# Kernel tuning notes

Hardware: AMD Instinct MI355X
Metric: run time of the kernel (lower is better)

## Reference

```python
import jax, jax.numpy as jnp
import numpy as np

N_NODES = 40000
N_EDGES = 640000
D_IN, D_HID, D_OUT = 128, 128, 40


def _gcn_layer(x, src, dst, norm, W, b, n):
    # PyG GCNConv: h = x @ W; aggregate norm * h[src] at dst; add bias.
    h = x @ W
    msg = norm[:, None] * h[src]          # [E+N, d] gathered messages
    return jax.ops.segment_sum(msg, dst, num_segments=n) + b


def setup_inputs() -> dict:
    key = jax.random.key(0)
    ks = jax.random.split(key, 8)
    x = jax.random.normal(ks[0], (N_NODES, D_IN), dtype=jnp.float32)
    edge_index = jax.random.randint(ks[1], (2, N_EDGES), 0, N_NODES)
    s_in = 1.0 / np.sqrt(D_IN)
    s_hid = 1.0 / np.sqrt(D_HID)
    W1 = jax.random.normal(ks[2], (D_IN, D_HID), dtype=jnp.float32) * s_in
    b1 = jnp.zeros((D_HID,), dtype=jnp.float32)
    W2 = jax.random.normal(ks[3], (D_HID, D_HID), dtype=jnp.float32) * s_hid
    b2 = jnp.zeros((D_HID,), dtype=jnp.float32)
    W3 = jax.random.normal(ks[4], (D_HID, D_OUT), dtype=jnp.float32) * s_hid
    b3 = jnp.zeros((D_OUT,), dtype=jnp.float32)
    return {"x": x, "edge_index": edge_index, "W1": W1, "b1": b1,
            "W2": W2, "b2": b2, "W3": W3, "b3": b3}


def reference(x, edge_index, W1, b1, W2, b2, W3, b3):
    n = x.shape[0]
    src = edge_index[0].astype(jnp.int32)
    dst = edge_index[1].astype(jnp.int32)

    # --- GCN normalization with self-loops (PyG GCNConv defaults) ---
    loops = jnp.arange(n, dtype=jnp.int32)
    src2 = jnp.concatenate([src, loops])
    dst2 = jnp.concatenate([dst, loops])
    deg = jax.ops.segment_sum(jnp.ones_like(dst2, dtype=x.dtype), dst2,
                              num_segments=n)
    dis = jnp.where(deg > 0, jax.lax.rsqrt(deg), 0.0)
    norm = dis[src2] * dis[dst2]          # [E+N]

    h = jax.nn.relu(_gcn_layer(x, src2, dst2, norm, W1, b1, n))
    h = jax.nn.relu(_gcn_layer(h, src2, dst2, norm, W2, b2, n))
    out = _gcn_layer(h, src2, dst2, norm, W3, b3, n)

    # --- reg_loss = trace(A @ A), A = dense COO adjacency (dupes summed) ---
    # trace(A@A) = sum_{i,j} A[i,j] * A[j,i]
    #            = sum over edge instances (i,j) of multiplicity of (j,i).
    # Computed sparsely via sorted key lookup instead of NxN densification.
    keys = src * n + dst                  # unique int32 key per (i,j)
    skeys = jnp.sort(keys)
    rev = dst * n + src
    lo = jnp.searchsorted(skeys, rev, side="left")
    hi = jnp.searchsorted(skeys, rev, side="right")
    reg_loss = jnp.sum((hi - lo).astype(jnp.float32))

    return jax.nn.log_softmax(out, axis=1), reg_loss
```

## Files before the change

kernel.cpp:

```cpp
#include <hip/hip_runtime.h>
#include <hip/hip_bf16.h>
#include <math.h>

#define NN 40000
#define EE 640000
#define CAP 64
#define MPAD 40064
#define LDS_STRIDE 136
#define FP8_STRIDE 144
#define E4B 625
#define NB 157

typedef short bf16x8 __attribute__((ext_vector_type(8)));
typedef float f32x16 __attribute__((ext_vector_type(16)));
typedef float f32x2 __attribute__((ext_vector_type(2)));

__device__ __forceinline__ unsigned bf16rne(float x) {
  unsigned u = __float_as_uint(x);
  return (u + 0x7fffu + ((u >> 16) & 1u)) >> 16;
}
__device__ __forceinline__ unsigned packbf2(float lo, float hi) {
  return bf16rne(lo) | (bf16rne(hi) << 16);
}
__device__ __forceinline__ float dis_of(const int* cnt, int i) {
  return rsqrtf((float)(cnt[i] + 1));
}
__device__ __forceinline__ f32x2 cvt2lo(unsigned u) {
  return __builtin_amdgcn_cvt_pk_f32_fp8((int)u, false);
}
__device__ __forceinline__ f32x2 cvt2hi(unsigned u) {
  return __builtin_amdgcn_cvt_pk_f32_fp8((int)u, true);
}
__device__ __forceinline__ unsigned char f32_to_fp8(float x) {
  return (unsigned char)(__builtin_amdgcn_cvt_pk_fp8_f32(x, x, 0, false) & 0xff);
}

__global__ __launch_bounds__(256) void edge_w_kernel(
    const int4* __restrict__ src4, const int4* __restrict__ dst4,
    int* __restrict__ cnt, unsigned short* __restrict__ csr,
    const float* __restrict__ W1, const float* __restrict__ W2,
    const float* __restrict__ W3, unsigned short* __restrict__ Wt1,
    unsigned short* __restrict__ Wt2, unsigned short* __restrict__ W3t,
    unsigned* __restrict__ Xb32, unsigned* __restrict__ H1b32) {
  int blk = blockIdx.x, t = threadIdx.x;
  if (blk < E4B) {
    int e = blk * 256 + t;
    int4 s = src4[e];
    int4 d = dst4[e];
    int p0 = atomicAdd(&cnt[d.x], 1);
    int p1 = atomicAdd(&cnt[d.y], 1);
    int p2 = atomicAdd(&cnt[d.z], 1);
    int p3 = atomicAdd(&cnt[d.w], 1);
    if (p0 < CAP) csr[d.x * CAP + p0] = (unsigned short)s.x;
    if (p1 < CAP) csr[d.y * CAP + p1] = (unsigned short)s.y;
    if (p2 < CAP) csr[d.z * CAP + p2] = (unsigned short)s.z;
    if (p3 < CAP) csr[d.w * CAP + p3] = (unsigned short)s.w;
  } else if (blk < 753) {
    bool is1 = blk < 689;
    int n = (blk - (is1 ? 625 : 689)) * 2 + (t >> 7);
    int k = t & 127;
    const float* W = is1 ? W1 : W2;
    unsigned short* Wt = is1 ? Wt1 : Wt2;
    Wt[n * 128 + k] = (unsigned short)bf16rne(W[k * 128 + n]);
  } else if (blk < 785) {
    int n = (blk - 753) * 2 + (t >> 7);
    int k = t & 127;
    float v = (n < 40) ? W3[k * 40 + n] : 0.f;
    W3t[n * 128 + k] = (unsigned short)bf16rne(v);
  } else {
    if (t < 32) Xb32[(size_t)NN * 32 + t] = 0u;
    else if (t < 64) H1b32[(size_t)NN * 32 + (t - 32)] = 0u;
  }
}

__global__ __launch_bounds__(256) void fill_x_kernel(
    const int* __restrict__ cnt, unsigned short* __restrict__ csr,
    const float4* __restrict__ X, uint2* __restrict__ Xb8v) {
  int blk = blockIdx.x, t = threadIdx.x;
  if (blk < NB) {
    int i = blk * 256 + t;
    if (i >= NN) return;
    int cn = cnt[i];
    cn = cn > CAP ? CAP : cn;
    int en = (cn + 7) & ~7;
    for (int k = cn; k < en; k++) csr[i * CAP + k] = (unsigned short)NN;
  } else {
    int i = (blk - NB) * 256 + t;
    float di = dis_of(cnt, i >> 4);
    float4 a = X[i * 2], b = X[i * 2 + 1];
    int lo = __builtin_amdgcn_cvt_pk_fp8_f32(di * a.x, di * a.y, 0, false);
    lo = __builtin_amdgcn_cvt_pk_fp8_f32(di * a.z, di * a.w, lo, true);
    int hi = __builtin_amdgcn_cvt_pk_fp8_f32(di * b.x, di * b.y, 0, false);
    hi = __builtin_amdgcn_cvt_pk_fp8_f32(di * b.z, di * b.w, hi, true);
    uint2 o;
    o.x = (unsigned)lo;
    o.y = (unsigned)hi;
    Xb8v[i] = o;
  }
}

__device__ __forceinline__ void agg128_body8(
    int node, int sub, const unsigned char* __restrict__ Hb,
    const int* __restrict__ cnt, const unsigned short* __restrict__ csr,
    unsigned* __restrict__ outB) {
  float di = dis_of(cnt, node);
  const unsigned char* Hbs = Hb + sub * 16;
  f32x2 a[8];
  {
    uint4 v = *(const uint4*)&Hbs[(size_t)node * 128];
    a[0] = cvt2lo(v.x);
    a[1] = cvt2hi(v.x);
    a[2] = cvt2lo(v.y);
    a[3] = cvt2hi(v.y);
    a[4] = cvt2lo(v.z);
    a[5] = cvt2hi(v.z);
    a[6] = cvt2lo(v.w);
    a[7] = cvt2hi(v.w);
  }
  int beg = node * CAP;
  int cn = cnt[node];
  cn = cn > CAP ? CAP : cn;
  int end = beg + ((cn + 7) & ~7);
  if (beg < end) {
    uint4 cs = *(const uint4*)&csr[beg];
    for (int e = beg; e < end; e += 8) {
      int s0 = cs.x & 0xffff, s1 = cs.x >> 16;
      int s2 = cs.y & 0xffff, s3 = cs.y >> 16;
      int s4 = cs.z & 0xffff, s5 = cs.z >> 16;
      int s6 = cs.w & 0xffff, s7 = cs.w >> 16;
      uint4 v0 = *(const uint4*)&Hbs[(size_t)s0 * 128];
      uint4 v1 = *(const uint4*)&Hbs[(size_t)s1 * 128];
      uint4 v2 = *(const uint4*)&Hbs[(size_t)s2 * 128];
      uint4 v3 = *(const uint4*)&Hbs[(size_t)s3 * 128];
      uint4 v4 = *(const uint4*)&Hbs[(size_t)s4 * 128];
      uint4 v5 = *(const uint4*)&Hbs[(size_t)s5 * 128];
      uint4 v6 = *(const uint4*)&Hbs[(size_t)s6 * 128];
      uint4 v7 = *(const uint4*)&Hbs[(size_t)s7 * 128];
      if (e + 8 < end) cs = *(const uint4*)&csr[e + 8];
#define ACC8(vv)                                    \
  a[0] += cvt2lo(vv.x); a[1] += cvt2hi(vv.x);       \
  a[2] += cvt2lo(vv.y); a[3] += cvt2hi(vv.y);       \
  a[4] += cvt2lo(vv.z); a[5] += cvt2hi(vv.z);       \
  a[6] += cvt2lo(vv.w); a[7] += cvt2hi(vv.w);
      ACC8(v0);
      ACC8(v1);
      ACC8(v2);
      ACC8(v3);
      ACC8(v4);
      ACC8(v5);
      ACC8(v6);
      ACC8(v7);
#undef ACC8
    }
  }
  unsigned o0 = packbf2(di * a[0].x, di * a[0].y);
  unsigned o1 = packbf2(di * a[1].x, di * a[1].y);
  unsigned o2 = packbf2(di * a[2].x, di * a[2].y);
  unsigned o3 = packbf2(di * a[3].x, di * a[3].y);
  unsigned o4 = packbf2(di * a[4].x, di * a[4].y);
  unsigned o5 = packbf2(di * a[5].x, di * a[5].y);
  unsigned o6 = packbf2(di * a[6].x, di * a[6].y);
  unsigned o7 = packbf2(di * a[7].x, di * a[7].y);
  *(uint4*)&outB[(size_t)node * 64 + sub * 8] = make_uint4(o0, o1, o2, o3);
  *(uint4*)&outB[(size_t)node * 64 + sub * 8 + 4] = make_uint4(o4, o5, o6, o7);
}

__global__ __launch_bounds__(256) void agg1_reg(
    const unsigned char* __restrict__ Xb8, const int* __restrict__ cnt,
    const unsigned short* __restrict__ csr, unsigned* __restrict__ outB,
    const int* __restrict__ src, const int* __restrict__ dst,
    float* __restrict__ out_scalar) {
  int blk = blockIdx.x, t = threadIdx.x;
  if (blk % 3 == 0) {
    int node = (blk / 3) * 32 + (t >> 3);
    agg128_body8(node, t & 7, Xb8, cnt, csr, outB);
    return;
  }
  int e = (blk - blk / 3 - 1) * 256 + t;
  int c = 0;
  {
    int i = src[e];
    unsigned j = (unsigned)dst[e];
    int cn = cnt[i];
    cn = cn > CAP ? CAP : cn;
    int q0 = (i * CAP) >> 3, q1 = q0 + (((cn + 7) & ~7) >> 3);
    const uint4* base = (const uint4*)csr;
    for (int q = q0; q < q1; q++) {
      uint4 v = base[q];
      c += ((v.x & 0xffffu) == j) + ((v.x >> 16) == j);
      c += ((v.y & 0xffffu) == j) + ((v.y >> 16) == j);
      c += ((v.z & 0xffffu) == j) + ((v.z >> 16) == j);
      c += ((v.w & 0xffffu) == j) + ((v.w >> 16) == j);
    }
  }
  float v = (float)c;
  for (int off = 32; off; off >>= 1) v += __shfl_down(v, off, 64);
  __shared__ float ws[4];
  int lane = threadIdx.x & 63, w = threadIdx.x >> 6;
  if (lane == 0) ws[w] = v;
  __syncthreads();
  if (threadIdx.x == 0) atomicAdd(out_scalar, ws[0] + ws[1] + ws[2] + ws[3]);
}

__global__ __launch_bounds__(256) void agg128b(
    const unsigned char* __restrict__ Hb8, const int* __restrict__ cnt,
    const unsigned short* __restrict__ csr, unsigned* __restrict__ outB) {
  int node = blockIdx.x * 32 + (threadIdx.x >> 3);
  agg128_body8(node, threadIdx.x & 7, Hb8, cnt, csr, outB);
}

__global__ __launch_bounds__(256) void gemm_mfma(
    const unsigned* __restrict__ Ab, const unsigned* __restrict__ Wt,
    const float* __restrict__ bias, const int* __restrict__ cnt,
    unsigned char* __restrict__ outB8) {
  __shared__ unsigned short At[128 * LDS_STRIDE];
  __shared__ unsigned short Bt[128 * LDS_STRIDE];
  __shared__ float dsh[128];
  int t = threadIdx.x;
  int rowBase = blockIdx.x * 128;
  if (t < 128) {
    int rr = rowBase + t;
    dsh[t] = (rr < NN) ? dis_of(cnt, rr) : 0.f;
  }
  {
    const uint4* ga = (const uint4*)(Ab + (size_t)rowBase * 64);
    const uint4* gw = (const uint4*)Wt;
#pragma unroll
    for (int i = 0; i < 8; i++) {
      int idx = i * 256 + t;
      int r = idx >> 4, c = idx & 15;
      uint4 va = ga[idx];
      uint4 vw = gw[idx];
      *(uint4*)&At[r * LDS_STRIDE + c * 8] = va;
      *(uint4*)&Bt[r * LDS_STRIDE + c * 8] = vw;
    }
  }
  __syncthreads();
  int lane = t & 63, w = t >> 6;
  int m31 = lane & 31;
  int khalf = (lane >> 5) * 8;
  f32x16 acc[4] = {};
#pragma unroll
  for (int ks = 0; ks < 8; ks++) {
    bf16x8 a = *(bf16x8*)&At[(w * 32 + m31) * LDS_STRIDE + ks * 16 + khalf];
#pragma unroll
    for (int nt = 0; nt < 4; nt++) {
      bf16x8 b = *(bf16x8*)&Bt[(nt * 32 + m31) * LDS_STRIDE + ks * 16 + khalf];
      acc[nt] = __builtin_amdgcn_mfma_f32_32x32x16_bf16(a, b, acc[nt], 0, 0, 0);
    }
  }
  __syncthreads();
  unsigned char* Ac = (unsigned char*)At;
  int rsel = (lane >> 5) * 4;
#pragma unroll
  for (int nt = 0; nt < 4; nt++) {
    int col = nt * 32 + m31;
    float bv = bias[col];
#pragma unroll
    for (int r = 0; r < 16; r++) {
      int rl = w * 32 + (r & 3) + 8 * (r >> 2) + rsel;
      float x = fmaxf(acc[nt][r] + bv, 0.f);
      Ac[rl * FP8_STRIDE + col] = f32_to_fp8(dsh[rl] * x);
    }
  }
  __syncthreads();
  {
#pragma unroll
    for (int i = 0; i < 4; i++) {
      int idx = i * 256 + t;
      int r = idx >> 3, c = idx & 7;
      int grow = rowBase + r;
      if (grow < NN) {
        uint4 vv = *(const uint4*)&Ac[r * FP8_STRIDE + c * 16];
        *(uint4*)&outB8[(size_t)grow * 128 + c * 16] = vv;
      }
    }
  }
}

__global__ __launch_bounds__(256) void gemm_mfma2(
    const unsigned* __restrict__ Ab, const unsigned* __restrict__ Wt,
    const float* __restrict__ bias, const int* __restrict__ cnt,
    const unsigned short* __restrict__ W3t, float* __restrict__ G3) {
  __shared__ unsigned short At[128 * LDS_STRIDE];
  __shared__ unsigned short Bt[128 * LDS_STRIDE];
  __shared__ float dsh[128];
  int t = threadIdx.x;
  int rowBase = blockIdx.x * 128;
  if (blockIdx.x == 0 && t < 40) G3[(size_t)NN * 40 + t] = 0.f;
  if (t < 128) {
    int rr = rowBase + t;
    dsh[t] = (rr < NN) ? dis_of(cnt, rr) : 0.f;
  }
  {
    const uint4* ga = (const uint4*)(Ab + (size_t)rowBase * 64);
    const uint4* gw = (const uint4*)Wt;
#pragma unroll
    for (int i = 0; i < 8; i++) {
      int idx = i * 256 + t;
      int r = idx >> 4, c = idx & 15;
      uint4 va = ga[idx];
      uint4 vw = gw[idx];
      *(uint4*)&At[r * LDS_STRIDE + c * 8] = va;
      *(uint4*)&Bt[r * LDS_STRIDE + c * 8] = vw;
    }
  }
  __syncthreads();
  int lane = t & 63, w = t >> 6;
  int m31 = lane & 31;
  int khalf = (lane >> 5) * 8;
  f32x16 acc[4] = {};
#pragma unroll
  for (int ks = 0; ks < 8; ks++) {
    bf16x8 a = *(bf16x8*)&At[(w * 32 + m31) * LDS_STRIDE + ks * 16 + khalf];
#pragma unroll
    for (int nt = 0; nt < 4; nt++) {
      bf16x8 b = *(bf16x8*)&Bt[(nt * 32 + m31) * LDS_STRIDE + ks * 16 + khalf];
      acc[nt] = __builtin_amdgcn_mfma_f32_32x32x16_bf16(a, b, acc[nt], 0, 0, 0);
    }
  }
  __syncthreads();
  int rsel = (lane >> 5) * 4;
#pragma unroll
  for (int nt = 0; nt < 4; nt++) {
    int col = nt * 32 + m31;
    float bv = bias[col];
#pragma unroll
    for (int r = 0; r < 16; r++) {
      int rl = w * 32 + (r & 3) + 8 * (r >> 2) + rsel;
      float x = fmaxf(acc[nt][r] + bv, 0.f);
      At[rl * LDS_STRIDE + col] = (unsigned short)bf16rne(dsh[rl] * x);
    }
  }
  {
    const uint4* gw3 = (const uint4*)W3t;
#pragma unroll
    for (int i = 0; i < 4; i++) {
      int idx = i * 256 + t;
      int r = idx >> 4, c = idx & 15;
      *(uint4*)&Bt[r * LDS_STRIDE + c * 8] = gw3[idx];
    }
  }
  __syncthreads();
  f32x16 acc2[2] = {};
#pragma unroll
  for (int ks = 0; ks < 8; ks++) {
    bf16x8 a = *(bf16x8*)&At[(w * 32 + m31) * LDS_STRIDE + ks * 16 + khalf];
#pragma unroll
    for (int nt = 0; nt < 2; nt++) {
      bf16x8 b = *(bf16x8*)&Bt[(nt * 32 + m31) * LDS_STRIDE + ks * 16 + khalf];
      acc2[nt] = __builtin_amdgcn_mfma_f32_32x32x16_bf16(a, b, acc2[nt], 0, 0, 0);
    }
  }
  __syncthreads();
  float* Gst = (float*)At;
#pragma unroll
  for (int nt = 0; nt < 2; nt++) {
    int col = nt * 32 + m31;
    if (col < 40) {
#pragma unroll
      for (int r = 0; r < 16; r++) {
        int rl = w * 32 + (r & 3) + 8 * (r >> 2) + rsel;
        Gst[rl * 40 + col] = acc2[nt][r];
      }
    }
  }
  __syncthreads();
  {
    int lim = NN - rowBase;
    int lim4 = (lim >= 128) ? 1280 : lim * 10;
#pragma unroll
    for (int i = 0; i < 5; i++) {
      int idx = i * 256 + t;
      if (idx < lim4) {
        float4 vv = *(const float4*)&Gst[idx * 4];
        *(float4*)&G3[(size_t)rowBase * 40 + idx * 4] = vv;
      }
    }
  }
}

__global__ __launch_bounds__(256) void agg40_softmax(
    const float* __restrict__ G, const int* __restrict__ cnt,
    const unsigned short* __restrict__ csr, const float* __restrict__ b3,
    float* __restrict__ outp) {
  int node = __builtin_amdgcn_readfirstlane(blockIdx.x * 4 + (threadIdx.x >> 6));
  int lane = threadIdx.x & 63;
  int cl = lane < 40 ? lane : 39;
  float di = dis_of(cnt, node);
  float a = G[(size_t)node * 40 + cl];
  int beg = node * CAP;
  int cn = cnt[node];
  cn = cn > CAP ? CAP : cn;
  int end = beg + ((cn + 7) & ~7);
  if (beg < end) {
    uint4 cs = *(const uint4*)&csr[beg];
    for (int e = beg; e < end; e += 8) {
      int s0 = cs.x & 0xffff, s1 = cs.x >> 16;
      int s2 = cs.y & 0xffff, s3 = cs.y >> 16;
      int s4 = cs.z & 0xffff, s5 = cs.z >> 16;
      int s6 = cs.w & 0xffff, s7 = cs.w >> 16;
      float g0 = G[(size_t)s0 * 40 + cl];
      float g1 = G[(size_t)s1 * 40 + cl];
      float g2 = G[(size_t)s2 * 40 + cl];
      float g3 = G[(size_t)s3 * 40 + cl];
      float g4 = G[(size_t)s4 * 40 + cl];
      float g5 = G[(size_t)s5 * 40 + cl];
      float g6 = G[(size_t)s6 * 40 + cl];
      float g7 = G[(size_t)s7 * 40 + cl];
      if (e + 8 < end) cs = *(const uint4*)&csr[e + 8];
      a += g0 + g1 + g2 + g3 + g4 + g5 + g6 + g7;
    }
  }
  float o = di * a + b3[cl];
  float m = (lane < 40) ? o : -1e30f;
  for (int off = 32; off; off >>= 1) m = fmaxf(m, __shfl_xor(m, off, 64));
  float ex = (lane < 40) ? expf(o - m) : 0.f;
  float ssum = ex;
  for (int off = 32; off; off >>= 1) ssum += __shfl_xor(ssum, off, 64);
  float res = o - m - logf(ssum);
  if (lane < 40) outp[(size_t)node * 40 + lane] = res;
}

extern "C" void kernel_launch(void* const* d_in, const int* in_sizes, int n_in,
                              void* d_out, int out_size, void* d_ws,
                              size_t ws_size, hipStream_t stream) {
  const float* X = (const float*)d_in[0];
  const int* ei = (const int*)d_in[1];
  const float* W1 = (const float*)d_in[2];
  const float* b1 = (const float*)d_in[3];
  const float* W2 = (const float*)d_in[4];
  const float* b2 = (const float*)d_in[5];
  const float* W3 = (const float*)d_in[6];
  const float* b3 = (const float*)d_in[7];
  float* out = (float*)d_out;

  const int* src = ei;
  const int* dst = ei + EE;

  char* w = (char*)d_ws;
  auto carve = [&](size_t bytes) {
    char* p = w;
    w += (bytes + 255) & ~(size_t)255;
    return p;
  };
  int* cnt = (int*)carve(NN * 4);
  unsigned short* csr = (unsigned short*)carve((size_t)NN * CAP * 2);
  unsigned short* Wt1 = (unsigned short*)carve(128 * 128 * 2);
  unsigned short* Wt2 = (unsigned short*)carve(128 * 128 * 2);
  unsigned short* W3t = (unsigned short*)carve(64 * 128 * 2);
  unsigned* Ab = (unsigned*)carve((size_t)MPAD * 128 * 2);
  char* blk = carve(((size_t)NN + 1) * 40 * 4 + ((size_t)NN + 1) * 128 * 2);
  unsigned char* Xb8 = (unsigned char*)blk;
  unsigned char* H1b8 = (unsigned char*)blk + ((size_t)NN + 1) * 128;
  float* G3 = (float*)blk;

  (void)hipMemsetAsync(cnt, 0, NN * 4, stream);
  (void)hipMemsetAsync((char*)d_out + (size_t)NN * 40 * 4, 0, 4, stream);

  const int GB = MPAD / 128;

  edge_w_kernel<<<786, 256, 0, stream>>>((const int4*)src, (const int4*)dst,
                                         cnt, csr, W1, W2, W3, Wt1, Wt2, W3t,
                                         (unsigned*)Xb8, (unsigned*)H1b8);
  fill_x_kernel<<<NB + 2500, 256, 0, stream>>>(cnt, csr, (const float4*)X,
                                               (uint2*)Xb8);
  agg1_reg<<<3750, 256, 0, stream>>>(Xb8, cnt, csr, Ab, src, dst,
                                     out + (size_t)NN * 40);
  gemm_mfma<<<GB, 256, 0, stream>>>(Ab, (const unsigned*)Wt1, b1, cnt, H1b8);
  agg128b<<<1250, 256, 0, stream>>>(H1b8, cnt, csr, Ab);
  gemm_mfma2<<<GB, 256, 0, stream>>>(Ab, (const unsigned*)Wt2, b2, cnt, W3t,
                                     G3);
  agg40_softmax<<<NN / 4, 256, 0, stream>>>(G3, cnt, csr, b3, out);
}
```

Baseline: 210.1 us.

## Split fp8 feature tables into column halves and restructure aggregation and reg-loss scheduling

Stores the fp8 node feature tables as two 64-byte column halves (A/B), and the aggregation kernel processes one half per block. Block indices are interleaved so groups of four blocks share a half, which should keep the gathered working set (about 2.5MB per half) cache-resident. CSR tail padding is replaced with in-loop masking to the dummy zero row, which removes the csr padding pass. The reg-loss edge counting moves into the fp8 conversion kernel, using masked tail handling. Outputs use nontemporal stores. In exchange there are more blocks, doubled index decode work per node, and extra select instructions.

```diff
diff --git a/kernel.cpp b/kernel.cpp
--- a/kernel.cpp
+++ b/kernel.cpp
@@ -9,11 +9,11 @@
 #define LDS_STRIDE 136
 #define FP8_STRIDE 144
 #define E4B 625
-#define NB 157
 
 typedef short bf16x8 __attribute__((ext_vector_type(8)));
 typedef float f32x16 __attribute__((ext_vector_type(16)));
 typedef float f32x2 __attribute__((ext_vector_type(2)));
+typedef unsigned u32x4 __attribute__((ext_vector_type(4)));
 
 __device__ __forceinline__ unsigned bf16rne(float x) {
   unsigned u = __float_as_uint(x);
@@ -41,7 +41,8 @@
     const float* __restrict__ W1, const float* __restrict__ W2,
     const float* __restrict__ W3, unsigned short* __restrict__ Wt1,
     unsigned short* __restrict__ Wt2, unsigned short* __restrict__ W3t,
-    unsigned* __restrict__ Xb32, unsigned* __restrict__ H1b32) {
+    unsigned* __restrict__ XbA32, unsigned* __restrict__ XbB32,
+    unsigned* __restrict__ HA32, unsigned* __restrict__ HB32) {
   int blk = blockIdx.x, t = threadIdx.x;
   if (blk < E4B) {
     int e = blk * 256 + t;
@@ -68,25 +69,23 @@
     float v = (n < 40) ? W3[k * 40 + n] : 0.f;
     W3t[n * 128 + k] = (unsigned short)bf16rne(v);
   } else {
-    if (t < 32) Xb32[(size_t)NN * 32 + t] = 0u;
-    else if (t < 64) H1b32[(size_t)NN * 32 + (t - 32)] = 0u;
+    if (t < 16) XbA32[(size_t)NN * 16 + t] = 0u;
+    else if (t < 32) XbB32[(size_t)NN * 16 + (t - 16)] = 0u;
+    else if (t < 48) HA32[(size_t)NN * 16 + (t - 32)] = 0u;
+    else if (t < 64) HB32[(size_t)NN * 16 + (t - 48)] = 0u;
   }
 }
 
 __global__ __launch_bounds__(256) void fill_x_kernel(
-    const int* __restrict__ cnt, unsigned short* __restrict__ csr,
-    const float4* __restrict__ X, uint2* __restrict__ Xb8v) {
+    const int* __restrict__ cnt, const float4* __restrict__ X,
+    uint2* __restrict__ XbA2, uint2* __restrict__ XbB2,
+    const unsigned short* __restrict__ csr, const int* __restrict__ src,
+    const int* __restrict__ dst, float* __restrict__ out_scalar) {
   int blk = blockIdx.x, t = threadIdx.x;
-  if (blk < NB) {
-    int i = blk * 256 + t;
-    if (i >= NN) return;
-    int cn = cnt[i];
-    cn = cn > CAP ? CAP : cn;
-    int en = (cn + 7) & ~7;
-    for (int k = cn; k < en; k++) csr[i * CAP + k] = (unsigned short)NN;
-  } else {
-    int i = (blk - NB) * 256 + t;
-    float di = dis_of(cnt, i >> 4);
+  if ((blk & 1) == 0) {
+    int i = (blk >> 1) * 256 + t;
+    int row = i >> 4, li = i & 15;
+    float di = dis_of(cnt, row);
     float4 a = X[i * 2], b = X[i * 2 + 1];
     int lo = __builtin_amdgcn_cvt_pk_fp8_f32(di * a.x, di * a.y, 0, false);
     lo = __builtin_amdgcn_cvt_pk_fp8_f32(di * a.z, di * a.w, lo, true);
@@ -95,103 +94,37 @@
     uint2 o;
     o.x = (unsigned)lo;
     o.y = (unsigned)hi;
-    Xb8v[i] = o;
-  }
-}
-
-__device__ __forceinline__ void agg128_body8(
-    int node, int sub, const unsigned char* __restrict__ Hb,
-    const int* __restrict__ cnt, const unsigned short* __restrict__ csr,
-    unsigned* __restrict__ outB) {
-  float di = dis_of(cnt, node);
-  const unsigned char* Hbs = Hb + sub * 16;
-  f32x2 a[8];
-  {
-    uint4 v = *(const uint4*)&Hbs[(size_t)node * 128];
-    a[0] = cvt2lo(v.x);
-    a[1] = cvt2hi(v.x);
-    a[2] = cvt2lo(v.y);
-    a[3] = cvt2hi(v.y);
-    a[4] = cvt2lo(v.z);
-    a[5] = cvt2hi(v.z);
-    a[6] = cvt2lo(v.w);
-    a[7] = cvt2hi(v.w);
-  }
-  int beg = node * CAP;
-  int cn = cnt[node];
-  cn = cn > CAP ? CAP : cn;
-  int end = beg + ((cn + 7) & ~7);
-  if (beg < end) {
-    uint4 cs = *(const uint4*)&csr[beg];
-    for (int e = beg; e < end; e += 8) {
-      int s0 = cs.x & 0xffff, s1 = cs.x >> 16;
-      int s2 = cs.y & 0xffff, s3 = cs.y >> 16;
-      int s4 = cs.z & 0xffff, s5 = cs.z >> 16;
-      int s6 = cs.w & 0xffff, s7 = cs.w >> 16;
-      uint4 v0 = *(const uint4*)&Hbs[(size_t)s0 * 128];
-      uint4 v1 = *(const uint4*)&Hbs[(size_t)s1 * 128];
-      uint4 v2 = *(const uint4*)&Hbs[(size_t)s2 * 128];
-      uint4 v3 = *(const uint4*)&Hbs[(size_t)s3 * 128];
-      uint4 v4 = *(const uint4*)&Hbs[(size_t)s4 * 128];
-      uint4 v5 = *(const uint4*)&Hbs[(size_t)s5 * 128];
-      uint4 v6 = *(const uint4*)&Hbs[(size_t)s6 * 128];
-      uint4 v7 = *(const uint4*)&Hbs[(size_t)s7 * 128];
-      if (e + 8 < end) cs = *(const uint4*)&csr[e + 8];
-#define ACC8(vv)                                    \
-  a[0] += cvt2lo(vv.x); a[1] += cvt2hi(vv.x);       \
-  a[2] += cvt2lo(vv.y); a[3] += cvt2hi(vv.y);       \
-  a[4] += cvt2lo(vv.z); a[5] += cvt2hi(vv.z);       \
-  a[6] += cvt2lo(vv.w); a[7] += cvt2hi(vv.w);
-      ACC8(v0);
-      ACC8(v1);
-      ACC8(v2);
-      ACC8(v3);
-      ACC8(v4);
-      ACC8(v5);
-      ACC8(v6);
-      ACC8(v7);
-#undef ACC8
-    }
-  }
-  unsigned o0 = packbf2(di * a[0].x, di * a[0].y);
-  unsigned o1 = packbf2(di * a[1].x, di * a[1].y);
-  unsigned o2 = packbf2(di * a[2].x, di * a[2].y);
-  unsigned o3 = packbf2(di * a[3].x, di * a[3].y);
-  unsigned o4 = packbf2(di * a[4].x, di * a[4].y);
-  unsigned o5 = packbf2(di * a[5].x, di * a[5].y);
-  unsigned o6 = packbf2(di * a[6].x, di * a[6].y);
-  unsigned o7 = packbf2(di * a[7].x, di * a[7].y);
-  *(uint4*)&outB[(size_t)node * 64 + sub * 8] = make_uint4(o0, o1, o2, o3);
-  *(uint4*)&outB[(size_t)node * 64 + sub * 8 + 4] = make_uint4(o4, o5, o6, o7);
-}
-
-__global__ __launch_bounds__(256) void agg1_reg(
-    const unsigned char* __restrict__ Xb8, const int* __restrict__ cnt,
-    const unsigned short* __restrict__ csr, unsigned* __restrict__ outB,
-    const int* __restrict__ src, const int* __restrict__ dst,
-    float* __restrict__ out_scalar) {
-  int blk = blockIdx.x, t = threadIdx.x;
-  if (blk % 3 == 0) {
-    int node = (blk / 3) * 32 + (t >> 3);
-    agg128_body8(node, t & 7, Xb8, cnt, csr, outB);
+    if (li < 8) XbA2[row * 8 + li] = o;
+    else XbB2[row * 8 + (li - 8)] = o;
     return;
   }
-  int e = (blk - blk / 3 - 1) * 256 + t;
+  int e = (blk >> 1) * 256 + t;
   int c = 0;
   {
     int i = src[e];
     unsigned j = (unsigned)dst[e];
     int cn = cnt[i];
     cn = cn > CAP ? CAP : cn;
-    int q0 = (i * CAP) >> 3, q1 = q0 + (((cn + 7) & ~7) >> 3);
-    const uint4* base = (const uint4*)csr;
-    for (int q = q0; q < q1; q++) {
+    const uint4* base = (const uint4*)&csr[i * CAP];
+    int full = cn >> 3;
+    for (int q = 0; q < full; q++) {
       uint4 v = base[q];
       c += ((v.x & 0xffffu) == j) + ((v.x >> 16) == j);
       c += ((v.y & 0xffffu) == j) + ((v.y >> 16) == j);
       c += ((v.z & 0xffffu) == j) + ((v.z >> 16) == j);
       c += ((v.w & 0xffffu) == j) + ((v.w >> 16) == j);
     }
+    int rem = cn & 7;
+    if (rem) {
+      uint4 v = base[full];
+      c += (int)((v.x & 0xffffu) == j);
+      c += ((v.x >> 16) == j) & (rem > 1);
+      c += ((v.y & 0xffffu) == j) & (rem > 2);
+      c += ((v.y >> 16) == j) & (rem > 3);
+      c += ((v.z & 0xffffu) == j) & (rem > 4);
+      c += ((v.z >> 16) == j) & (rem > 5);
+      c += ((v.w & 0xffffu) == j) & (rem > 6);
+    }
   }
   float v = (float)c;
   for (int off = 32; off; off >>= 1) v += __shfl_down(v, off, 64);
@@ -202,17 +135,81 @@
   if (threadIdx.x == 0) atomicAdd(out_scalar, ws[0] + ws[1] + ws[2] + ws[3]);
 }
 
-__global__ __launch_bounds__(256) void agg128b(
-    const unsigned char* __restrict__ Hb8, const int* __restrict__ cnt,
-    const unsigned short* __restrict__ csr, unsigned* __restrict__ outB) {
-  int node = blockIdx.x * 32 + (threadIdx.x >> 3);
-  agg128_body8(node, threadIdx.x & 7, Hb8, cnt, csr, outB);
+__global__ __launch_bounds__(256) void agg64(
+    const unsigned char* __restrict__ TA, const unsigned char* __restrict__ TB,
+    const int* __restrict__ cnt, const unsigned short* __restrict__ csr,
+    unsigned* __restrict__ outB) {
+  int blk = blockIdx.x, t = threadIdx.x;
+  int r = blk & 7;
+  int half = (r >> 2) & 1;
+  int nb = (blk >> 3) * 4 + (r & 3);
+  if (nb >= 1250) return;
+  int node = nb * 32 + (t >> 3);
+  int sub = t & 7;
+  const unsigned char* Hbs = (half ? TB : TA) + sub * 8;
+  float di = dis_of(cnt, node);
+  f32x2 a0, a1, a2, a3;
+  {
+    uint2 v = *(const uint2*)&Hbs[(size_t)node * 64];
+    a0 = cvt2lo(v.x);
+    a1 = cvt2hi(v.x);
+    a2 = cvt2lo(v.y);
+    a3 = cvt2hi(v.y);
+  }
+  int cn = cnt[node];
+  cn = cn > CAP ? CAP : cn;
+  const unsigned short* row = &csr[node * CAP];
+  if (cn > 0) {
+    uint4 cs = *(const uint4*)row;
+    for (int e = 0; e < cn; e += 8) {
+      int rem = cn - e;
+      int s0 = cs.x & 0xffff, s1 = cs.x >> 16;
+      int s2 = cs.y & 0xffff, s3 = cs.y >> 16;
+      int s4 = cs.z & 0xffff, s5 = cs.z >> 16;
+      int s6 = cs.w & 0xffff, s7 = cs.w >> 16;
+      s1 = rem > 1 ? s1 : NN;
+      s2 = rem > 2 ? s2 : NN;
+      s3 = rem > 3 ? s3 : NN;
+      s4 = rem > 4 ? s4 : NN;
+      s5 = rem > 5 ? s5 : NN;
+      s6 = rem > 6 ? s6 : NN;
+      s7 = rem > 7 ? s7 : NN;
+      uint2 v0 = *(const uint2*)&Hbs[(size_t)s0 * 64];
+      uint2 v1 = *(const uint2*)&Hbs[(size_t)s1 * 64];
+      uint2 v2 = *(const uint2*)&Hbs[(size_t)s2 * 64];
+      uint2 v3 = *(const uint2*)&Hbs[(size_t)s3 * 64];
+      uint2 v4 = *(const uint2*)&Hbs[(size_t)s4 * 64];
+      uint2 v5 = *(const uint2*)&Hbs[(size_t)s5 * 64];
+      uint2 v6 = *(const uint2*)&Hbs[(size_t)s6 * 64];
+      uint2 v7 = *(const uint2*)&Hbs[(size_t)s7 * 64];
+      if (e + 8 < cn) cs = *(const uint4*)&row[e + 8];
+#define ACC2(vv)                                    \
+  a0 += cvt2lo(vv.x); a1 += cvt2hi(vv.x);           \
+  a2 += cvt2lo(vv.y); a3 += cvt2hi(vv.y);
+      ACC2(v0);
+      ACC2(v1);
+      ACC2(v2);
+      ACC2(v3);
+      ACC2(v4);
+      ACC2(v5);
+      ACC2(v6);
+      ACC2(v7);
+#undef ACC2
+    }
+  }
+  u32x4 o;
+  o.x = packbf2(di * a0.x, di * a0.y);
+  o.y = packbf2(di * a1.x, di * a1.y);
+  o.z = packbf2(di * a2.x, di * a2.y);
+  o.w = packbf2(di * a3.x, di * a3.y);
+  __builtin_nontemporal_store(
+      o, (u32x4*)&outB[(size_t)node * 64 + half * 32 + sub * 4]);
 }
 
 __global__ __launch_bounds__(256) void gemm_mfma(
     const unsigned* __restrict__ Ab, const unsigned* __restrict__ Wt,
     const float* __restrict__ bias, const int* __restrict__ cnt,
-    unsigned char* __restrict__ outB8) {
+    unsigned char* __restrict__ HA8, unsigned char* __restrict__ HB8) {
   __shared__ unsigned short At[128 * LDS_STRIDE];
   __shared__ unsigned short Bt[128 * LDS_STRIDE];
   __shared__ float dsh[128];
@@ -272,7 +269,10 @@
       int grow = rowBase + r;
       if (grow < NN) {
         uint4 vv = *(const uint4*)&Ac[r * FP8_STRIDE + c * 16];
-        *(uint4*)&outB8[(size_t)grow * 128 + c * 16] = vv;
+        if (c < 4)
+          *(uint4*)&HA8[(size_t)grow * 64 + c * 16] = vv;
+        else
+          *(uint4*)&HB8[(size_t)grow * 64 + (c - 4) * 16] = vv;
       }
     }
   }
@@ -389,17 +389,24 @@
   int cl = lane < 40 ? lane : 39;
   float di = dis_of(cnt, node);
   float a = G[(size_t)node * 40 + cl];
-  int beg = node * CAP;
   int cn = cnt[node];
   cn = cn > CAP ? CAP : cn;
-  int end = beg + ((cn + 7) & ~7);
-  if (beg < end) {
-    uint4 cs = *(const uint4*)&csr[beg];
-    for (int e = beg; e < end; e += 8) {
+  const unsigned short* row = &csr[node * CAP];
+  if (cn > 0) {
+    uint4 cs = *(const uint4*)row;
+    for (int e = 0; e < cn; e += 8) {
+      int rem = cn - e;
       int s0 = cs.x & 0xffff, s1 = cs.x >> 16;
       int s2 = cs.y & 0xffff, s3 = cs.y >> 16;
       int s4 = cs.z & 0xffff, s5 = cs.z >> 16;
       int s6 = cs.w & 0xffff, s7 = cs.w >> 16;
+      s1 = rem > 1 ? s1 : NN;
+      s2 = rem > 2 ? s2 : NN;
+      s3 = rem > 3 ? s3 : NN;
+      s4 = rem > 4 ? s4 : NN;
+      s5 = rem > 5 ? s5 : NN;
+      s6 = rem > 6 ? s6 : NN;
+      s7 = rem > 7 ? s7 : NN;
       float g0 = G[(size_t)s0 * 40 + cl];
       float g1 = G[(size_t)s1 * 40 + cl];
       float g2 = G[(size_t)s2 * 40 + cl];
@@ -408,7 +415,7 @@
       float g5 = G[(size_t)s5 * 40 + cl];
       float g6 = G[(size_t)s6 * 40 + cl];
       float g7 = G[(size_t)s7 * 40 + cl];
-      if (e + 8 < end) cs = *(const uint4*)&csr[e + 8];
+      if (e + 8 < cn) cs = *(const uint4*)&row[e + 8];
       a += g0 + g1 + g2 + g3 + g4 + g5 + g6 + g7;
     }
   }
@@ -450,25 +457,26 @@
   unsigned short* Wt2 = (unsigned short*)carve(128 * 128 * 2);
   unsigned short* W3t = (unsigned short*)carve(64 * 128 * 2);
   unsigned* Ab = (unsigned*)carve((size_t)MPAD * 128 * 2);
-  char* blk = carve(((size_t)NN + 1) * 40 * 4 + ((size_t)NN + 1) * 128 * 2);
-  unsigned char* Xb8 = (unsigned char*)blk;
-  unsigned char* H1b8 = (unsigned char*)blk + ((size_t)NN + 1) * 128;
-  float* G3 = (float*)blk;
+  unsigned char* XbA = (unsigned char*)carve(((size_t)NN + 1) * 64);
+  unsigned char* XbB = (unsigned char*)carve(((size_t)NN + 1) * 64);
+  unsigned char* HA = (unsigned char*)carve(((size_t)NN + 1) * 64);
+  unsigned char* HB = (unsigned char*)carve(((size_t)NN + 1) * 64);
+  float* G3 = (float*)carve(((size_t)NN + 1) * 40 * 4);
 
   (void)hipMemsetAsync(cnt, 0, NN * 4, stream);
   (void)hipMemsetAsync((char*)d_out + (size_t)NN * 40 * 4, 0, 4, stream);
 
   const int GB = MPAD / 128;
 
-  edge_w_kernel<<<786, 256, 0, stream>>>((const int4*)src, (const int4*)dst,
-                                         cnt, csr, W1, W2, W3, Wt1, Wt2, W3t,
-                                         (unsigned*)Xb8, (unsigned*)H1b8);
-  fill_x_kernel<<<NB + 2500, 256, 0, stream>>>(cnt, csr, (const float4*)X,
-                                               (uint2*)Xb8);
-  agg1_reg<<<3750, 256, 0, stream>>>(Xb8, cnt, csr, Ab, src, dst,
-                                     out + (size_t)NN * 40);
-  gemm_mfma<<<GB, 256, 0, stream>>>(Ab, (const unsigned*)Wt1, b1, cnt, H1b8);
-  agg128b<<<1250, 256, 0, stream>>>(H1b8, cnt, csr, Ab);
+  edge_w_kernel<<<786, 256, 0, stream>>>(
+      (const int4*)src, (const int4*)dst, cnt, csr, W1, W2, W3, Wt1, Wt2, W3t,
+      (unsigned*)XbA, (unsigned*)XbB, (unsigned*)HA, (unsigned*)HB);
+  fill_x_kernel<<<5000, 256, 0, stream>>>(cnt, (const float4*)X, (uint2*)XbA,
+                                          (uint2*)XbB, csr, src, dst,
+                                          out + (size_t)NN * 40);
+  agg64<<<2504, 256, 0, stream>>>(XbA, XbB, cnt, csr, Ab);
+  gemm_mfma<<<GB, 256, 0, stream>>>(Ab, (const unsigned*)Wt1, b1, cnt, HA, HB);
+  agg64<<<2504, 256, 0, stream>>>(HA, HB, cnt, csr, Ab);
   gemm_mfma2<<<GB, 256, 0, stream>>>(Ab, (const unsigned*)Wt2, b2, cnt, W3t,
                                      G3);
   agg40_softmax<<<NN / 4, 256, 0, stream>>>(G3, cnt, csr, b3, out);
```

New measurement: 217.6 us. 1.04x slower.

## Drop CSR padding pass and split reg-loss counting across two aggregation kernels

Applied to the files above, without the earlier changes.

Removes the per-node pass that padded each CSR row to a multiple of eight with a sentinel index. Instead, the aggregation loops mask the tail slots in registers by redirecting them to the zero sentinel row, and the reg-loss count masks the tail comparisons. The reg-loss edge counting is also split in half: the first half is interleaved with layer-1 aggregation and the second half with layer-2 aggregation, which replaces the separate agg128b kernel. This trims a write pass over the CSR and balances the extra work between two launches, at the cost of a few more selects in the inner loops.

```diff
diff --git a/kernel.cpp b/kernel.cpp
--- a/kernel.cpp
+++ b/kernel.cpp
@@ -9,7 +9,6 @@
 #define LDS_STRIDE 136
 #define FP8_STRIDE 144
 #define E4B 625
-#define NB 157
 
 typedef short bf16x8 __attribute__((ext_vector_type(8)));
 typedef float f32x16 __attribute__((ext_vector_type(16)));
@@ -74,29 +73,19 @@
 }
 
 __global__ __launch_bounds__(256) void fill_x_kernel(
-    const int* __restrict__ cnt, unsigned short* __restrict__ csr,
-    const float4* __restrict__ X, uint2* __restrict__ Xb8v) {
-  int blk = blockIdx.x, t = threadIdx.x;
-  if (blk < NB) {
-    int i = blk * 256 + t;
-    if (i >= NN) return;
-    int cn = cnt[i];
-    cn = cn > CAP ? CAP : cn;
-    int en = (cn + 7) & ~7;
-    for (int k = cn; k < en; k++) csr[i * CAP + k] = (unsigned short)NN;
-  } else {
-    int i = (blk - NB) * 256 + t;
-    float di = dis_of(cnt, i >> 4);
-    float4 a = X[i * 2], b = X[i * 2 + 1];
-    int lo = __builtin_amdgcn_cvt_pk_fp8_f32(di * a.x, di * a.y, 0, false);
-    lo = __builtin_amdgcn_cvt_pk_fp8_f32(di * a.z, di * a.w, lo, true);
-    int hi = __builtin_amdgcn_cvt_pk_fp8_f32(di * b.x, di * b.y, 0, false);
-    hi = __builtin_amdgcn_cvt_pk_fp8_f32(di * b.z, di * b.w, hi, true);
-    uint2 o;
-    o.x = (unsigned)lo;
-    o.y = (unsigned)hi;
-    Xb8v[i] = o;
-  }
+    const int* __restrict__ cnt, const float4* __restrict__ X,
+    uint2* __restrict__ Xb8v) {
+  int i = blockIdx.x * 256 + threadIdx.x;
+  float di = dis_of(cnt, i >> 4);
+  float4 a = X[i * 2], b = X[i * 2 + 1];
+  int lo = __builtin_amdgcn_cvt_pk_fp8_f32(di * a.x, di * a.y, 0, false);
+  lo = __builtin_amdgcn_cvt_pk_fp8_f32(di * a.z, di * a.w, lo, true);
+  int hi = __builtin_amdgcn_cvt_pk_fp8_f32(di * b.x, di * b.y, 0, false);
+  hi = __builtin_amdgcn_cvt_pk_fp8_f32(di * b.z, di * b.w, hi, true);
+  uint2 o;
+  o.x = (unsigned)lo;
+  o.y = (unsigned)hi;
+  Xb8v[i] = o;
 }
 
 __device__ __forceinline__ void agg128_body8(
@@ -105,29 +94,36 @@
     unsigned* __restrict__ outB) {
   float di = dis_of(cnt, node);
   const unsigned char* Hbs = Hb + sub * 16;
-  f32x2 a[8];
+  f32x2 a0, a1, a2, a3, a4, a5, a6, a7;
   {
     uint4 v = *(const uint4*)&Hbs[(size_t)node * 128];
-    a[0] = cvt2lo(v.x);
-    a[1] = cvt2hi(v.x);
-    a[2] = cvt2lo(v.y);
-    a[3] = cvt2hi(v.y);
-    a[4] = cvt2lo(v.z);
-    a[5] = cvt2hi(v.z);
-    a[6] = cvt2lo(v.w);
-    a[7] = cvt2hi(v.w);
-  }
-  int beg = node * CAP;
+    a0 = cvt2lo(v.x);
+    a1 = cvt2hi(v.x);
+    a2 = cvt2lo(v.y);
+    a3 = cvt2hi(v.y);
+    a4 = cvt2lo(v.z);
+    a5 = cvt2hi(v.z);
+    a6 = cvt2lo(v.w);
+    a7 = cvt2hi(v.w);
+  }
   int cn = cnt[node];
   cn = cn > CAP ? CAP : cn;
-  int end = beg + ((cn + 7) & ~7);
-  if (beg < end) {
-    uint4 cs = *(const uint4*)&csr[beg];
-    for (int e = beg; e < end; e += 8) {
+  const unsigned short* row = &csr[node * CAP];
+  if (cn > 0) {
+    uint4 cs = *(const uint4*)row;
+    for (int e = 0; e < cn; e += 8) {
+      int rem = cn - e;
       int s0 = cs.x & 0xffff, s1 = cs.x >> 16;
       int s2 = cs.y & 0xffff, s3 = cs.y >> 16;
       int s4 = cs.z & 0xffff, s5 = cs.z >> 16;
       int s6 = cs.w & 0xffff, s7 = cs.w >> 16;
+      s1 = rem > 1 ? s1 : NN;
+      s2 = rem > 2 ? s2 : NN;
+      s3 = rem > 3 ? s3 : NN;
+      s4 = rem > 4 ? s4 : NN;
+      s5 = rem > 5 ? s5 : NN;
+      s6 = rem > 6 ? s6 : NN;
+      s7 = rem > 7 ? s7 : NN;
       uint4 v0 = *(const uint4*)&Hbs[(size_t)s0 * 128];
       uint4 v1 = *(const uint4*)&Hbs[(size_t)s1 * 128];
       uint4 v2 = *(const uint4*)&Hbs[(size_t)s2 * 128];
@@ -136,12 +132,12 @@
       uint4 v5 = *(const uint4*)&Hbs[(size_t)s5 * 128];
       uint4 v6 = *(const uint4*)&Hbs[(size_t)s6 * 128];
       uint4 v7 = *(const uint4*)&Hbs[(size_t)s7 * 128];
-      if (e + 8 < end) cs = *(const uint4*)&csr[e + 8];
+      if (e + 8 < cn) cs = *(const uint4*)&row[e + 8];
 #define ACC8(vv)                                    \
-  a[0] += cvt2lo(vv.x); a[1] += cvt2hi(vv.x);       \
-  a[2] += cvt2lo(vv.y); a[3] += cvt2hi(vv.y);       \
-  a[4] += cvt2lo(vv.z); a[5] += cvt2hi(vv.z);       \
-  a[6] += cvt2lo(vv.w); a[7] += cvt2hi(vv.w);
+  a0 += cvt2lo(vv.x); a1 += cvt2hi(vv.x);           \
+  a2 += cvt2lo(vv.y); a3 += cvt2hi(vv.y);           \
+  a4 += cvt2lo(vv.z); a5 += cvt2hi(vv.z);           \
+  a6 += cvt2lo(vv.w); a7 += cvt2hi(vv.w);
       ACC8(v0);
       ACC8(v1);
       ACC8(v2);
@@ -153,45 +149,56 @@
 #undef ACC8
     }
   }
-  unsigned o0 = packbf2(di * a[0].x, di * a[0].y);
-  unsigned o1 = packbf2(di * a[1].x, di * a[1].y);
-  unsigned o2 = packbf2(di * a[2].x, di * a[2].y);
-  unsigned o3 = packbf2(di * a[3].x, di * a[3].y);
-  unsigned o4 = packbf2(di * a[4].x, di * a[4].y);
-  unsigned o5 = packbf2(di * a[5].x, di * a[5].y);
-  unsigned o6 = packbf2(di * a[6].x, di * a[6].y);
-  unsigned o7 = packbf2(di * a[7].x, di * a[7].y);
+  unsigned o0 = packbf2(di * a0.x, di * a0.y);
+  unsigned o1 = packbf2(di * a1.x, di * a1.y);
+  unsigned o2 = packbf2(di * a2.x, di * a2.y);
+  unsigned o3 = packbf2(di * a3.x, di * a3.y);
+  unsigned o4 = packbf2(di * a4.x, di * a4.y);
+  unsigned o5 = packbf2(di * a5.x, di * a5.y);
+  unsigned o6 = packbf2(di * a6.x, di * a6.y);
+  unsigned o7 = packbf2(di * a7.x, di * a7.y);
   *(uint4*)&outB[(size_t)node * 64 + sub * 8] = make_uint4(o0, o1, o2, o3);
   *(uint4*)&outB[(size_t)node * 64 + sub * 8 + 4] = make_uint4(o4, o5, o6, o7);
 }
 
-__global__ __launch_bounds__(256) void agg1_reg(
-    const unsigned char* __restrict__ Xb8, const int* __restrict__ cnt,
+__global__ __launch_bounds__(256) void agg_reg(
+    const unsigned char* __restrict__ Hb8, const int* __restrict__ cnt,
     const unsigned short* __restrict__ csr, unsigned* __restrict__ outB,
-    const int* __restrict__ src, const int* __restrict__ dst,
+    const int* __restrict__ src, const int* __restrict__ dst, int ebase,
     float* __restrict__ out_scalar) {
   int blk = blockIdx.x, t = threadIdx.x;
-  if (blk % 3 == 0) {
-    int node = (blk / 3) * 32 + (t >> 3);
-    agg128_body8(node, t & 7, Xb8, cnt, csr, outB);
+  if ((blk & 1) == 0) {
+    int node = (blk >> 1) * 32 + (t >> 3);
+    agg128_body8(node, t & 7, Hb8, cnt, csr, outB);
     return;
   }
-  int e = (blk - blk / 3 - 1) * 256 + t;
+  int e = ebase + (blk >> 1) * 256 + t;
   int c = 0;
   {
     int i = src[e];
     unsigned j = (unsigned)dst[e];
     int cn = cnt[i];
     cn = cn > CAP ? CAP : cn;
-    int q0 = (i * CAP) >> 3, q1 = q0 + (((cn + 7) & ~7) >> 3);
-    const uint4* base = (const uint4*)csr;
-    for (int q = q0; q < q1; q++) {
+    const uint4* base = (const uint4*)&csr[i * CAP];
+    int full = cn >> 3;
+    for (int q = 0; q < full; q++) {
       uint4 v = base[q];
       c += ((v.x & 0xffffu) == j) + ((v.x >> 16) == j);
       c += ((v.y & 0xffffu) == j) + ((v.y >> 16) == j);
       c += ((v.z & 0xffffu) == j) + ((v.z >> 16) == j);
       c += ((v.w & 0xffffu) == j) + ((v.w >> 16) == j);
     }
+    int rem = cn & 7;
+    if (rem) {
+      uint4 v = base[full];
+      c += (int)((v.x & 0xffffu) == j);
+      c += ((v.x >> 16) == j) & (rem > 1);
+      c += ((v.y & 0xffffu) == j) & (rem > 2);
+      c += ((v.y >> 16) == j) & (rem > 3);
+      c += ((v.z & 0xffffu) == j) & (rem > 4);
+      c += ((v.z >> 16) == j) & (rem > 5);
+      c += ((v.w & 0xffffu) == j) & (rem > 6);
+    }
   }
   float v = (float)c;
   for (int off = 32; off; off >>= 1) v += __shfl_down(v, off, 64);
@@ -200,13 +207,6 @@
   if (lane == 0) ws[w] = v;
   __syncthreads();
   if (threadIdx.x == 0) atomicAdd(out_scalar, ws[0] + ws[1] + ws[2] + ws[3]);
-}
-
-__global__ __launch_bounds__(256) void agg128b(
-    const unsigned char* __restrict__ Hb8, const int* __restrict__ cnt,
-    const unsigned short* __restrict__ csr, unsigned* __restrict__ outB) {
-  int node = blockIdx.x * 32 + (threadIdx.x >> 3);
-  agg128_body8(node, threadIdx.x & 7, Hb8, cnt, csr, outB);
 }
 
 __global__ __launch_bounds__(256) void gemm_mfma(
@@ -389,17 +389,24 @@
   int cl = lane < 40 ? lane : 39;
   float di = dis_of(cnt, node);
   float a = G[(size_t)node * 40 + cl];
-  int beg = node * CAP;
   int cn = cnt[node];
   cn = cn > CAP ? CAP : cn;
-  int end = beg + ((cn + 7) & ~7);
-  if (beg < end) {
-    uint4 cs = *(const uint4*)&csr[beg];
-    for (int e = beg; e < end; e += 8) {
+  const unsigned short* row = &csr[node * CAP];
+  if (cn > 0) {
+    uint4 cs = *(const uint4*)row;
+    for (int e = 0; e < cn; e += 8) {
+      int rem = cn - e;
       int s0 = cs.x & 0xffff, s1 = cs.x >> 16;
       int s2 = cs.y & 0xffff, s3 = cs.y >> 16;
       int s4 = cs.z & 0xffff, s5 = cs.z >> 16;
       int s6 = cs.w & 0xffff, s7 = cs.w >> 16;
+      s1 = rem > 1 ? s1 : NN;
+      s2 = rem > 2 ? s2 : NN;
+      s3 = rem > 3 ? s3 : NN;
+      s4 = rem > 4 ? s4 : NN;
+      s5 = rem > 5 ? s5 : NN;
+      s6 = rem > 6 ? s6 : NN;
+      s7 = rem > 7 ? s7 : NN;
       float g0 = G[(size_t)s0 * 40 + cl];
       float g1 = G[(size_t)s1 * 40 + cl];
       float g2 = G[(size_t)s2 * 40 + cl];
@@ -408,7 +415,7 @@
       float g5 = G[(size_t)s5 * 40 + cl];
       float g6 = G[(size_t)s6 * 40 + cl];
       float g7 = G[(size_t)s7 * 40 + cl];
-      if (e + 8 < end) cs = *(const uint4*)&csr[e + 8];
+      if (e + 8 < cn) cs = *(const uint4*)&row[e + 8];
       a += g0 + g1 + g2 + g3 + g4 + g5 + g6 + g7;
     }
   }
@@ -463,12 +470,12 @@
   edge_w_kernel<<<786, 256, 0, stream>>>((const int4*)src, (const int4*)dst,
                                          cnt, csr, W1, W2, W3, Wt1, Wt2, W3t,
                                          (unsigned*)Xb8, (unsigned*)H1b8);
-  fill_x_kernel<<<NB + 2500, 256, 0, stream>>>(cnt, csr, (const float4*)X,
-                                               (uint2*)Xb8);
-  agg1_reg<<<3750, 256, 0, stream>>>(Xb8, cnt, csr, Ab, src, dst,
-                                     out + (size_t)NN * 40);
+  fill_x_kernel<<<2500, 256, 0, stream>>>(cnt, (const float4*)X, (uint2*)Xb8);
+  agg_reg<<<2500, 256, 0, stream>>>(Xb8, cnt, csr, Ab, src, dst, 0,
+                                    out + (size_t)NN * 40);
   gemm_mfma<<<GB, 256, 0, stream>>>(Ab, (const unsigned*)Wt1, b1, cnt, H1b8);
-  agg128b<<<1250, 256, 0, stream>>>(H1b8, cnt, csr, Ab);
+  agg_reg<<<2500, 256, 0, stream>>>(H1b8, cnt, csr, Ab, src, dst, EE / 2,
+                                    out + (size_t)NN * 40);
   gemm_mfma2<<<GB, 256, 0, stream>>>(Ab, (const unsigned*)Wt2, b2, cnt, W3t,
                                      G3);
   agg40_softmax<<<NN / 4, 256, 0, stream>>>(G3, cnt, csr, b3, out);
```

Result: faster. 204.4 us (-2.7%).
